# Kernel tuning notes

Measured on AMD Instinct MI355X. Metric: run time of the kernel, lower is better.

The kernel has to match this reference:

```python
import jax, jax.numpy as jnp
import numpy as np
import math

FACTOR = 5


def setup_inputs() -> dict:
    key = jax.random.key(0)
    k1, k2, k3, k4 = jax.random.split(key, 4)
    B, L, H, D = 8, 1024, 8, 64
    S = FACTOR * math.ceil(math.log(L))  # U_part = 35
    return {
        "queries": jax.random.normal(k1, (B, L, H, D), jnp.float32),
        "keys": jax.random.normal(k2, (B, L, H, D), jnp.float32),
        "values": jax.random.normal(k3, (B, L, H, D), jnp.float32),
        "sample_idx": jax.random.randint(k4, (L, S), 0, L, dtype=jnp.int32),
        "attn_mask": 0,  # unused by the original forward
    }


def reference(queries, keys, values, sample_idx, attn_mask):
    B, L_Q, H, D = queries.shape
    L_K = keys.shape[1]
    # [B, L, H, D] -> [B, H, L, D]
    Q = jnp.transpose(queries, (0, 2, 1, 3))
    K = jnp.transpose(keys, (0, 2, 1, 3))
    V = jnpp_transpose(values) if False else jnp.transpose(values, (0, 2, 1, 3))

    u = min(FACTOR * math.ceil(math.log(L_Q)), L_Q)  # n_top

    # --- _prob_QK: sampled scores, sparsity measure, top-u query selection ---
    K_sample = K[:, :, sample_idx, :]  # [B, H, L_Q, S, D]
    QK_sample = jnp.einsum('bhqd,bhqsd->bhqs', Q, K_sample)  # [B, H, L_Q, S]
    M = QK_sample.max(axis=-1) - QK_sample.sum(axis=-1) / L_K  # [B, H, L_Q]
    _, M_top = jax.lax.top_k(M, u)  # [B, H, u]

    Q_reduce = jnp.take_along_axis(Q, M_top[..., None], axis=2)  # [B, H, u, D]
    scale = 1.0 / math.sqrt(D)
    scores_top = jnp.einsum('bhud,bhkd->bhuk', Q_reduce, K) * scale  # [B, H, u, L_K]

    # --- initial context (mask_flag=True): running causal mean of V ---
    denom = jnp.arange(1, L_K + 1, dtype=V.dtype)[:, None]  # [L_K, 1]
    context = jnp.cumsum(V, axis=2) / denom  # [B, H, L_K, D]

    # --- softmax over keys, sparse update of selected query rows ---
    attn = jax.nn.softmax(scores_top, axis=-1)  # [B, H, u, L_K]
    update = jnp.einsum('bhuk,bhkd->bhud', attn, V)  # [B, H, u, D]

    b_idx = jnp.arange(B)[:, None, None]
    h_idx = jnp.arange(H)[None, :, None]
    context = context.at[b_idx, h_idx, M_top].set(update)

    return jnp.transpose(context, (0, 2, 1, 3))  # [B, L_Q, H, D]
```

## Files before the change

### kernel.cpp

```cpp
#include <hip/hip_runtime.h>
#include <math.h>

#define BB 8
#define LL 1024
#define HH 8
#define DD 64
#define SS 35
#define UU 35
#define BH (BB*HH)
#define NCHK 4
#define CHK 256
#define RPAD 48

#define CSBLOCKS BH
#define MBLOCKS (BB*LL)

typedef __attribute__((ext_vector_type(8))) short short8;
typedef __attribute__((ext_vector_type(4))) float f32x4;

__device__ __forceinline__ size_t qkv_off(int b, int l, int h, int d) {
    return (((size_t)b*LL + l)*HH + h)*DD + d;
}

__device__ __forceinline__ unsigned short f2bf(float x) {
    unsigned int u = __float_as_uint(x);
    u = (u + 0x7fffu + ((u >> 16) & 1u)) >> 16;
    return (unsigned short)u;
}

__device__ __forceinline__ short8 ld_bf8_g(const float* __restrict__ p) {
    float4 x = *reinterpret_cast<const float4*>(p);
    float4 y = *reinterpret_cast<const float4*>(p + 4);
    short8 r;
    r[0] = (short)f2bf(x.x); r[1] = (short)f2bf(x.y);
    r[2] = (short)f2bf(x.z); r[3] = (short)f2bf(x.w);
    r[4] = (short)f2bf(y.x); r[5] = (short)f2bf(y.y);
    r[6] = (short)f2bf(y.z); r[7] = (short)f2bf(y.w);
    return r;
}

__device__ __forceinline__ float red8_shr(float p) {
    int t;
    t = __builtin_amdgcn_update_dpp(0, __float_as_int(p), 0x111, 0xF, 0xF, true);
    p += __int_as_float(t);
    t = __builtin_amdgcn_update_dpp(0, __float_as_int(p), 0x112, 0xF, 0xF, true);
    p += __int_as_float(t);
    t = __builtin_amdgcn_update_dpp(0, __float_as_int(p), 0x114, 0xF, 0xF, true);
    p += __int_as_float(t);
    return p;
}

__device__ __forceinline__ float wave_fmax64(float x) {
    int t;
    t = __builtin_amdgcn_update_dpp(0, __float_as_int(x), 0xB1, 0xF, 0xF, true);
    x = fmaxf(x, __int_as_float(t));
    t = __builtin_amdgcn_update_dpp(0, __float_as_int(x), 0x4E, 0xF, 0xF, true);
    x = fmaxf(x, __int_as_float(t));
    t = __builtin_amdgcn_update_dpp(0, __float_as_int(x), 0x141, 0xF, 0xF, true);
    x = fmaxf(x, __int_as_float(t));
    t = __builtin_amdgcn_update_dpp(0, __float_as_int(x), 0x140, 0xF, 0xF, true);
    x = fmaxf(x, __int_as_float(t));
    x = fmaxf(x, __shfl_xor(x, 16));
    x = fmaxf(x, __shfl_xor(x, 32));
    return x;
}

__device__ __forceinline__ int wave_imin64(int x) {
    int t;
    t = __builtin_amdgcn_update_dpp(0, x, 0xB1, 0xF, 0xF, true);  x = (t < x) ? t : x;
    t = __builtin_amdgcn_update_dpp(0, x, 0x4E, 0xF, 0xF, true);  x = (t < x) ? t : x;
    t = __builtin_amdgcn_update_dpp(0, x, 0x141, 0xF, 0xF, true); x = (t < x) ? t : x;
    t = __builtin_amdgcn_update_dpp(0, x, 0x140, 0xF, 0xF, true); x = (t < x) ? t : x;
    int y;
    y = __shfl_xor(x, 16); x = (y < x) ? y : x;
    y = __shfl_xor(x, 32); x = (y < x) ? y : x;
    return x;
}

__global__ __launch_bounds__(512, 2) void kernel_M_cumsum(const float* __restrict__ Q,
                                                          const float* __restrict__ K,
                                                          const float* __restrict__ V,
                                                          const int*   __restrict__ sidx,
                                                          float* __restrict__ M,
                                                          float* __restrict__ out) {
    int blk = blockIdx.x;
    if (blk < CSBLOCKS) {
        __shared__ float partial[8][64];
        int bh = blk;
        int b = bh >> 3, h = bh & 7;
        int d = threadIdx.x & 63, seg = threadIdx.x >> 6;
        int l0 = seg * 128;
        const float* vp = V + qkv_off(b, l0, h, d);

        float s = 0.f;
#pragma unroll 8
        for (int i = 0; i < 128; i++) s += vp[(size_t)i * (HH * DD)];
        partial[seg][d] = s;
        __syncthreads();
        float run = 0.f;
#pragma unroll
        for (int ss = 0; ss < 7; ss++) {
            float v = partial[ss][d];
            run += (ss < seg) ? v : 0.f;
        }
        float* op = out + qkv_off(b, l0, h, d);
#pragma unroll 8
        for (int i = 0; i < 128; i++) {
            run += vp[(size_t)i * (HH * DD)];
            op[(size_t)i * (HH * DD)] = run / (float)(l0 + i + 1);
        }
    } else {
        __shared__ float s_mx[8][8];
        __shared__ float s_sm[8][8];
        int mblk = blk - CSBLOCKS;
        int b = mblk & 7;
        int q = mblk >> 3;
        int tid = threadIdx.x;
        int w = tid >> 6, lane = tid & 63;
        int h = lane >> 3, j = lane & 7, dsub = j * 4;

        const float* qb = Q + ((size_t)(b * LL + q) * HH + h) * DD + dsub;
        f32x4 q0 = *reinterpret_cast<const f32x4*>(qb);
        f32x4 q1 = *reinterpret_cast<const f32x4*>(qb + 32);

        const int* sq = sidx + q * SS;
        int s0i = w, s1i = w + 8, s2i = w + 16, s3i = w + 24, s4i = (w + 32 < SS) ? w + 32 : 0;
        int sl0 = sq[s0i], sl1 = sq[s1i], sl2 = sq[s2i], sl3 = sq[s3i], sl4 = sq[s4i];

        const float* kbase = K + (size_t)b * (LL * HH * DD) + h * DD + dsub;
        const float* kp0 = kbase + (size_t)sl0 * (HH * DD);
        const float* kp1 = kbase + (size_t)sl1 * (HH * DD);
        const float* kp2 = kbase + (size_t)sl2 * (HH * DD);
        const float* kp3 = kbase + (size_t)sl3 * (HH * DD);
        const float* kp4 = kbase + (size_t)sl4 * (HH * DD);

        f32x4 a0, a1, a2, a3, a4, c0, c1, c2, c3, c4;
        asm volatile("global_load_dwordx4 %0, %1, off"            : "=v"(a0) : "v"(kp0));
        asm volatile("global_load_dwordx4 %0, %1, off offset:128" : "=v"(c0) : "v"(kp0));
        asm volatile("global_load_dwordx4 %0, %1, off"            : "=v"(a1) : "v"(kp1));
        asm volatile("global_load_dwordx4 %0, %1, off offset:128" : "=v"(c1) : "v"(kp1));
        asm volatile("global_load_dwordx4 %0, %1, off"            : "=v"(a2) : "v"(kp2));
        asm volatile("global_load_dwordx4 %0, %1, off offset:128" : "=v"(c2) : "v"(kp2));
        asm volatile("global_load_dwordx4 %0, %1, off"            : "=v"(a3) : "v"(kp3));
        asm volatile("global_load_dwordx4 %0, %1, off offset:128" : "=v"(c3) : "v"(kp3));
        asm volatile("global_load_dwordx4 %0, %1, off"            : "=v"(a4) : "v"(kp4));
        asm volatile("global_load_dwordx4 %0, %1, off offset:128" : "=v"(c4) : "v"(kp4));
        asm volatile("s_waitcnt vmcnt(0)" ::: "memory");
        __builtin_amdgcn_sched_barrier(0);

        float mx = -INFINITY, sm = 0.f;
        {
            float d0 = q0.x * a0.x + q0.y * a0.y + q0.z * a0.z + q0.w * a0.w
                     + q1.x * c0.x + q1.y * c0.y + q1.z * c0.z + q1.w * c0.w;
            d0 = red8_shr(d0);
            mx = fmaxf(mx, d0); sm += d0;
            float d1 = q0.x * a1.x + q0.y * a1.y + q0.z * a1.z + q0.w * a1.w
                     + q1.x * c1.x + q1.y * c1.y + q1.z * c1.z + q1.w * c1.w;
            d1 = red8_shr(d1);
            mx = fmaxf(mx, d1); sm += d1;
            float d2 = q0.x * a2.x + q0.y * a2.y + q0.z * a2.z + q0.w * a2.w
                     + q1.x * c2.x + q1.y * c2.y + q1.z * c2.z + q1.w * c2.w;
            d2 = red8_shr(d2);
            mx = fmaxf(mx, d2); sm += d2;
            float d3 = q0.x * a3.x + q0.y * a3.y + q0.z * a3.z + q0.w * a3.w
                     + q1.x * c3.x + q1.y * c3.y + q1.z * c3.z + q1.w * c3.w;
            d3 = red8_shr(d3);
            mx = fmaxf(mx, d3); sm += d3;
            float d4 = q0.x * a4.x + q0.y * a4.y + q0.z * a4.z + q0.w * a4.w
                     + q1.x * c4.x + q1.y * c4.y + q1.z * c4.z + q1.w * c4.w;
            d4 = red8_shr(d4);
            bool valid = (w < 3);
            mx = fmaxf(mx, valid ? d4 : -INFINITY);
            sm += valid ? d4 : 0.f;
        }

        if (j == 7) { s_mx[w][h] = mx; s_sm[w][h] = sm; }
        __syncthreads();
        if (tid < 8) {
            float m2 = -INFINITY, s2 = 0.f;
#pragma unroll
            for (int ww = 0; ww < 8; ww++) {
                m2 = fmaxf(m2, s_mx[ww][tid]);
                s2 += s_sm[ww][tid];
            }
            M[(b * HH + tid) * LL + q] = m2 - s2 * (1.0f / LL);
        }
    }
}

__global__ __launch_bounds__(256) void kernel_attn_part(const float* __restrict__ Q,
                                                        const float* __restrict__ K,
                                                        const float* __restrict__ V,
                                                        const float* __restrict__ M,
                                                        int*   __restrict__ top,
                                                        float* __restrict__ m_ws,
                                                        float* __restrict__ se_ws,
                                                        float* __restrict__ pv_ws) {
    __shared__ unsigned short vt[64 * CHK];
    __shared__ unsigned short p_lds[RPAD * CHK];
    __shared__ float red_m[4][RPAD];
    __shared__ float red_se[4][RPAD];
    __shared__ int   qpos_s[RPAD];

    const int blk = blockIdx.x;
    const int bh  = blk >> 2;
    const int ch  = blk & 3;
    const int b   = bh >> 3, h = bh & 7;
    const int l0  = ch * CHK;
    const int tid = threadIdx.x;
    const int w    = tid >> 6;
    const int lane = tid & 63;
    const int c    = lane & 15;
    const int g    = lane >> 4;
    const float scale = 0.125f;

    if (w == 0) {
        float v[16];
#pragma unroll
        for (int i = 0; i < 16; i++) v[i] = M[bh * LL + i * 64 + lane];
        int last = 0;
        for (int k = 0; k < UU; k++) {
            float bv = -INFINITY; int bslot = 0;
#pragma unroll
            for (int i = 0; i < 16; i++) {
                if (v[i] > bv) { bv = v[i]; bslot = i; }
            }
            float wm = wave_fmax64(bv);
            int gidx = (bv == wm) ? (bslot * 64 + lane) : 0x7fffffff;
            int widx = wave_imin64(gidx);
            if (lane == 0) qpos_s[k] = widx;
            if (k == UU - 1) last = widx;
            if ((widx & 63) == lane) {
                int slot = widx >> 6;
#pragma unroll
                for (int i = 0; i < 16; i++) if (i == slot) v[i] = -INFINITY;
            }
        }
        if (lane >= UU && lane < RPAD) qpos_s[lane] = last;
        if (ch == 0 && lane < UU) top[bh * UU + lane] = qpos_s[lane];
    } else {
        int t3 = tid - 64;
#pragma unroll
        for (int i = 0; i < 11; i++) {
            int task = i * 192 + t3;
            if (task < 2048) {
                int d   = task & 63;
                int lq8 = task >> 6;
                float vv[8];
#pragma unroll
                for (int jj = 0; jj < 8; jj++)
                    vv[jj] = V[qkv_off(b, l0 + lq8 * 8 + jj, h, d)];
                short8 pk;
#pragma unroll
                for (int jj = 0; jj < 8; jj++) pk[jj] = (short)f2bf(vv[jj]);
                *reinterpret_cast<short8*>(vt + d * CHK + (((lq8 ^ (d & 31)) << 3))) = pk;
            }
        }
    }
    __syncthreads();

    f32x4 acc[3][4];
#pragma unroll
    for (int mt = 0; mt < 3; mt++)
#pragma unroll
        for (int nt = 0; nt < 4; nt++) acc[mt][nt] = (f32x4){0.f, 0.f, 0.f, 0.f};

#pragma unroll
    for (int ks = 0; ks < 2; ks++) {
        int k0 = ks * 32 + g * 8;
        short8 af[3];
#pragma unroll
        for (int mt = 0; mt < 3; mt++) {
            int row = mt * 16 + c;
            af[mt] = ld_bf8_g(Q + qkv_off(b, qpos_s[row], h, k0));
        }
#pragma unroll
        for (int nt = 0; nt < 4; nt++) {
            int kl = l0 + w * 64 + nt * 16 + c;
            short8 bf = ld_bf8_g(K + qkv_off(b, kl, h, k0));
#pragma unroll
            for (int mt = 0; mt < 3; mt++)
                acc[mt][nt] = __builtin_amdgcn_mfma_f32_16x16x32_bf16(af[mt], bf, acc[mt][nt], 0, 0, 0);
        }
    }

    float tmax[3][4];
#pragma unroll
    for (int mt = 0; mt < 3; mt++)
#pragma unroll
        for (int r = 0; r < 4; r++) {
            float m = fmaxf(fmaxf(acc[mt][0][r], acc[mt][1][r]),
                            fmaxf(acc[mt][2][r], acc[mt][3][r]));
            m = fmaxf(m, __shfl_xor(m, 1));
            m = fmaxf(m, __shfl_xor(m, 2));
            m = fmaxf(m, __shfl_xor(m, 4));
            m = fmaxf(m, __shfl_xor(m, 8));
            tmax[mt][r] = m;
        }
    if (c == 0) {
#pragma unroll
        for (int mt = 0; mt < 3; mt++)
#pragma unroll
            for (int r = 0; r < 4; r++)
                red_m[w][mt * 16 + g * 4 + r] = tmax[mt][r];
    }
    __syncthreads();

    float tse[3][4];
#pragma unroll
    for (int mt = 0; mt < 3; mt++)
#pragma unroll
        for (int r = 0; r < 4; r++) {
            int row = mt * 16 + g * 4 + r;
            float m = fmaxf(fmaxf(red_m[0][row], red_m[1][row]),
                            fmaxf(red_m[2][row], red_m[3][row]));
            float s = 0.f;
#pragma unroll
            for (int nt = 0; nt < 4; nt++) {
                float p = __expf(scale * (acc[mt][nt][r] - m));
                acc[mt][nt][r] = p;
                s += p;
                p_lds[row * CHK + w * 64 + nt * 16 + c] = f2bf(p);
            }
            s += __shfl_xor(s, 1);
            s += __shfl_xor(s, 2);
            s += __shfl_xor(s, 4);
            s += __shfl_xor(s, 8);
            tse[mt][r] = s;
        }
    if (c == 0) {
#pragma unroll
        for (int mt = 0; mt < 3; mt++)
#pragma unroll
            for (int r = 0; r < 4; r++)
                red_se[w][mt * 16 + g * 4 + r] = tse[mt][r];
    }
    __syncthreads();

    if (tid < RPAD) {
        float mm = fmaxf(fmaxf(red_m[0][tid], red_m[1][tid]),
                         fmaxf(red_m[2][tid], red_m[3][tid]));
        float ss = red_se[0][tid] + red_se[1][tid] + red_se[2][tid] + red_se[3][tid];
        m_ws[blk * RPAD + tid]  = mm;
        se_ws[blk * RPAD + tid] = ss;
    }

    f32x4 acc2[3];
#pragma unroll
    for (int mt = 0; mt < 3; mt++) acc2[mt] = (f32x4){0.f, 0.f, 0.f, 0.f};

#pragma unroll
    for (int ks = 0; ks < 8; ks++) {
        int slot = ks * 4 + g;
        int d    = w * 16 + c;
        short8 bf = *reinterpret_cast<const short8*>(
            vt + d * CHK + ((slot ^ (d & 31)) << 3));
#pragma unroll
        for (int mt = 0; mt < 3; mt++) {
            short8 af = *reinterpret_cast<const short8*>(
                p_lds + (mt * 16 + c) * CHK + ks * 32 + g * 8);
            acc2[mt] = __builtin_amdgcn_mfma_f32_16x16x32_bf16(af, bf, acc2[mt], 0, 0, 0);
        }
    }

#pragma unroll
    for (int mt = 0; mt < 3; mt++)
#pragma unroll
        for (int r = 0; r < 4; r++) {
            int row = mt * 16 + g * 4 + r;
            pv_ws[((size_t)blk * RPAD + row) * 64 + w * 16 + c] = acc2[mt][r];
        }
}

__global__ __launch_bounds__(256) void kernel_attn_comb(const int* __restrict__ top,
                                                        const float* __restrict__ m_ws,
                                                        const float* __restrict__ se_ws,
                                                        const float* __restrict__ pv_ws,
                                                        float* __restrict__ out) {
    int bh = blockIdx.x;
    int b = bh >> 3, h = bh & 7;
    const float scale = 0.125f;
    for (int idx = threadIdx.x; idx < UU * 64; idx += 256) {
        int r = idx >> 6, d = idx & 63;
        float mc[NCHK];
        float mm = -INFINITY;
#pragma unroll
        for (int ch = 0; ch < NCHK; ch++) {
            mc[ch] = m_ws[(bh * NCHK + ch) * RPAD + r];
            mm = fmaxf(mm, mc[ch]);
        }
        float num = 0.f, den = 0.f;
#pragma unroll
        for (int ch = 0; ch < NCHK; ch++) {
            float f = __expf(scale * (mc[ch] - mm));
            num += f * pv_ws[((size_t)(bh * NCHK + ch) * RPAD + r) * 64 + d];
            den += f * se_ws[(bh * NCHK + ch) * RPAD + r];
        }
        out[qkv_off(b, top[bh * UU + r], h, d)] = num / den;
    }
}

extern "C" void kernel_launch(void* const* d_in, const int* in_sizes, int n_in,
                              void* d_out, int out_size, void* d_ws, size_t ws_size,
                              hipStream_t stream) {
    const float* Q    = (const float*)d_in[0];
    const float* K    = (const float*)d_in[1];
    const float* V    = (const float*)d_in[2];
    const int*   sidx = (const int*)d_in[3];
    float* out = (float*)d_out;

    char* ws = (char*)d_ws;
    float* M     = (float*)(ws);
    int*   top   = (int*)  (ws + 262144);
    float* m_ws  = (float*)(ws + 272384);
    float* se_ws = (float*)(ws + 321536);
    float* pv_ws = (float*)(ws + 370688);

    kernel_M_cumsum <<<CSBLOCKS + MBLOCKS, 512, 0, stream>>>(Q, K, V, sidx, M, out);
    kernel_attn_part<<<BH * NCHK, 256, 0, stream>>>(Q, K, V, M, top, m_ws, se_ws, pv_ws);
    kernel_attn_comb<<<BH, 256, 0, stream>>>(top, m_ws, se_ws, pv_ws, out);
}
```

Baseline: 68.46 us.

## Fuse chunk-combine into attention kernel via last-block atomic counter

Removes the separate combine kernel: each attention-part block increments a per-(b,h) atomic counter, and the last of the four chunk blocks merges the partial softmax results and scatters the selected rows into the output, using its own shared top-k positions. A memset resets the counters before each launch. The fifth sampled-key load in the M kernel is now predicated so waves without a fifth sample skip that gather. This trades one kernel launch and the global top-index buffer for threadfences, an atomic and a serial tail in the last block.

Result: slower. 107.5 us (+57.1%).

```diff
diff --git a/kernel.cpp b/kernel.cpp
--- a/kernel.cpp
+++ b/kernel.cpp
@@ -124,17 +124,15 @@
         f32x4 q1 = *reinterpret_cast<const f32x4*>(qb + 32);
 
         const int* sq = sidx + q * SS;
-        int s0i = w, s1i = w + 8, s2i = w + 16, s3i = w + 24, s4i = (w + 32 < SS) ? w + 32 : 0;
-        int sl0 = sq[s0i], sl1 = sq[s1i], sl2 = sq[s2i], sl3 = sq[s3i], sl4 = sq[s4i];
+        int sl0 = sq[w], sl1 = sq[w + 8], sl2 = sq[w + 16], sl3 = sq[w + 24];
 
         const float* kbase = K + (size_t)b * (LL * HH * DD) + h * DD + dsub;
         const float* kp0 = kbase + (size_t)sl0 * (HH * DD);
         const float* kp1 = kbase + (size_t)sl1 * (HH * DD);
         const float* kp2 = kbase + (size_t)sl2 * (HH * DD);
         const float* kp3 = kbase + (size_t)sl3 * (HH * DD);
-        const float* kp4 = kbase + (size_t)sl4 * (HH * DD);
-
-        f32x4 a0, a1, a2, a3, a4, c0, c1, c2, c3, c4;
+
+        f32x4 a0, a1, a2, a3, c0, c1, c2, c3, a4, c4;
         asm volatile("global_load_dwordx4 %0, %1, off"            : "=v"(a0) : "v"(kp0));
         asm volatile("global_load_dwordx4 %0, %1, off offset:128" : "=v"(c0) : "v"(kp0));
         asm volatile("global_load_dwordx4 %0, %1, off"            : "=v"(a1) : "v"(kp1));
@@ -143,8 +141,12 @@
         asm volatile("global_load_dwordx4 %0, %1, off offset:128" : "=v"(c2) : "v"(kp2));
         asm volatile("global_load_dwordx4 %0, %1, off"            : "=v"(a3) : "v"(kp3));
         asm volatile("global_load_dwordx4 %0, %1, off offset:128" : "=v"(c3) : "v"(kp3));
-        asm volatile("global_load_dwordx4 %0, %1, off"            : "=v"(a4) : "v"(kp4));
-        asm volatile("global_load_dwordx4 %0, %1, off offset:128" : "=v"(c4) : "v"(kp4));
+        bool have5 = (w < 3);
+        if (have5) {
+            const float* kp4 = kbase + (size_t)sq[w + 32] * (HH * DD);
+            asm volatile("global_load_dwordx4 %0, %1, off"            : "=v"(a4) : "v"(kp4));
+            asm volatile("global_load_dwordx4 %0, %1, off offset:128" : "=v"(c4) : "v"(kp4));
+        }
         asm volatile("s_waitcnt vmcnt(0)" ::: "memory");
         __builtin_amdgcn_sched_barrier(0);
 
@@ -166,12 +168,12 @@
                      + q1.x * c3.x + q1.y * c3.y + q1.z * c3.z + q1.w * c3.w;
             d3 = red8_shr(d3);
             mx = fmaxf(mx, d3); sm += d3;
-            float d4 = q0.x * a4.x + q0.y * a4.y + q0.z * a4.z + q0.w * a4.w
-                     + q1.x * c4.x + q1.y * c4.y + q1.z * c4.z + q1.w * c4.w;
-            d4 = red8_shr(d4);
-            bool valid = (w < 3);
-            mx = fmaxf(mx, valid ? d4 : -INFINITY);
-            sm += valid ? d4 : 0.f;
+            if (have5) {
+                float d4 = q0.x * a4.x + q0.y * a4.y + q0.z * a4.z + q0.w * a4.w
+                         + q1.x * c4.x + q1.y * c4.y + q1.z * c4.z + q1.w * c4.w;
+                d4 = red8_shr(d4);
+                mx = fmaxf(mx, d4); sm += d4;
+            }
         }
 
         if (j == 7) { s_mx[w][h] = mx; s_sm[w][h] = sm; }
@@ -192,15 +194,17 @@
                                                         const float* __restrict__ K,
                                                         const float* __restrict__ V,
                                                         const float* __restrict__ M,
-                                                        int*   __restrict__ top,
                                                         float* __restrict__ m_ws,
                                                         float* __restrict__ se_ws,
-                                                        float* __restrict__ pv_ws) {
+                                                        float* __restrict__ pv_ws,
+                                                        int*   __restrict__ cnt,
+                                                        float* __restrict__ out) {
     __shared__ unsigned short vt[64 * CHK];
     __shared__ unsigned short p_lds[RPAD * CHK];
     __shared__ float red_m[4][RPAD];
     __shared__ float red_se[4][RPAD];
     __shared__ int   qpos_s[RPAD];
+    __shared__ int   s_done;
 
     const int blk = blockIdx.x;
     const int bh  = blk >> 2;
@@ -237,7 +241,6 @@
             }
         }
         if (lane >= UU && lane < RPAD) qpos_s[lane] = last;
-        if (ch == 0 && lane < UU) top[bh * UU + lane] = qpos_s[lane];
     } else {
         int t3 = tid - 64;
 #pragma unroll
@@ -370,33 +373,34 @@
             int row = mt * 16 + g * 4 + r;
             pv_ws[((size_t)blk * RPAD + row) * 64 + w * 16 + c] = acc2[mt][r];
         }
-}
-
-__global__ __launch_bounds__(256) void kernel_attn_comb(const int* __restrict__ top,
-                                                        const float* __restrict__ m_ws,
-                                                        const float* __restrict__ se_ws,
-                                                        const float* __restrict__ pv_ws,
-                                                        float* __restrict__ out) {
-    int bh = blockIdx.x;
-    int b = bh >> 3, h = bh & 7;
-    const float scale = 0.125f;
-    for (int idx = threadIdx.x; idx < UU * 64; idx += 256) {
-        int r = idx >> 6, d = idx & 63;
-        float mc[NCHK];
-        float mm = -INFINITY;
-#pragma unroll
-        for (int ch = 0; ch < NCHK; ch++) {
-            mc[ch] = m_ws[(bh * NCHK + ch) * RPAD + r];
-            mm = fmaxf(mm, mc[ch]);
-        }
-        float num = 0.f, den = 0.f;
-#pragma unroll
-        for (int ch = 0; ch < NCHK; ch++) {
-            float f = __expf(scale * (mc[ch] - mm));
-            num += f * pv_ws[((size_t)(bh * NCHK + ch) * RPAD + r) * 64 + d];
-            den += f * se_ws[(bh * NCHK + ch) * RPAD + r];
-        }
-        out[qkv_off(b, top[bh * UU + r], h, d)] = num / den;
+
+    __threadfence();
+    __syncthreads();
+    if (tid == 0) {
+        int old = atomicAdd(&cnt[bh], 1);
+        s_done = (old == NCHK - 1);
+    }
+    __syncthreads();
+    if (s_done) {
+        __threadfence();
+        for (int idx = tid; idx < UU * 64; idx += 256) {
+            int r = idx >> 6, d = idx & 63;
+            float mc[NCHK];
+            float mm = -INFINITY;
+#pragma unroll
+            for (int c2 = 0; c2 < NCHK; c2++) {
+                mc[c2] = m_ws[(bh * NCHK + c2) * RPAD + r];
+                mm = fmaxf(mm, mc[c2]);
+            }
+            float num = 0.f, den = 0.f;
+#pragma unroll
+            for (int c2 = 0; c2 < NCHK; c2++) {
+                float f = __expf(scale * (mc[c2] - mm));
+                num += f * pv_ws[((size_t)(bh * NCHK + c2) * RPAD + r) * 64 + d];
+                den += f * se_ws[(bh * NCHK + c2) * RPAD + r];
+            }
+            out[qkv_off(b, qpos_s[r], h, d)] = num / den;
+        }
     }
 }
 
@@ -411,12 +415,12 @@
 
     char* ws = (char*)d_ws;
     float* M     = (float*)(ws);
-    int*   top   = (int*)  (ws + 262144);
+    int*   cnt   = (int*)  (ws + 262144);
     float* m_ws  = (float*)(ws + 272384);
     float* se_ws = (float*)(ws + 321536);
     float* pv_ws = (float*)(ws + 370688);
 
+    hipMemsetAsync(cnt, 0, BH * sizeof(int), stream);
     kernel_M_cumsum <<<CSBLOCKS + MBLOCKS, 512, 0, stream>>>(Q, K, V, sidx, M, out);
-    kernel_attn_part<<<BH * NCHK, 256, 0, stream>>>(Q, K, V, M, top, m_ws, se_ws, pv_ws);
-    kernel_attn_comb<<<BH, 256, 0, stream>>>(top, m_ws, se_ws, pv_ws, out);
-}
+    kernel_attn_part<<<BH * NCHK, 256, 0, stream>>>(Q, K, V, M, m_ws, se_ws, pv_ws, cnt, out);
+}
```
